# Kernel optimization log

Hardware: AMD Instinct MI355X
Metric: run time of the kernel (lower is better)

## Reference

```python
import jax, jax.numpy as jnp
import numpy as np

HIDDEN = 512
HEADS = 8
HEAD_DIM = HIDDEN // HEADS
INNER = int(HIDDEN * 4.0)
MAX_DIST = 512
LN_EPS = 1e-5


def _layernorm(x, g, b):
    mu = jnp.mean(x, axis=-1, keepdims=True)
    var = jnp.var(x, axis=-1, keepdims=True)
    return (x - mu) * jax.lax.rsqrt(var + LN_EPS) * g + b


def setup_inputs() -> dict:
    key = jax.random.key(0)
    ks = jax.random.split(key, 12)
    B, T = 4, 2048
    s = 0.02
    return {
        "x": jax.random.normal(ks[0], (B, T, HIDDEN), dtype=jnp.float32),
        "w_qkv": jax.random.normal(ks[1], (HIDDEN, 3 * HIDDEN), dtype=jnp.float32) * s,
        "b_qkv": jnp.zeros((3 * HIDDEN,), dtype=jnp.float32),
        "w_out": jax.random.normal(ks[2], (HIDDEN, HIDDEN), dtype=jnp.float32) * s,
        "b_out": jnp.zeros((HIDDEN,), dtype=jnp.float32),
        "ln1_g": jnp.ones((HIDDEN,), dtype=jnp.float32),
        "ln1_b": jnp.zeros((HIDDEN,), dtype=jnp.float32),
        "ln2_g": jnp.ones((HIDDEN,), dtype=jnp.float32),
        "ln2_b": jnp.zeros((HIDDEN,), dtype=jnp.float32),
        "w_mlp1": jax.random.normal(ks[3], (HIDDEN, INNER), dtype=jnp.float32) * s,
        "b_mlp1": jnp.zeros((INNER,), dtype=jnp.float32),
        "w_mlp2": jax.random.normal(ks[4], (INNER, HIDDEN), dtype=jnp.float32) * s,
        "b_mlp2": jnp.zeros((HIDDEN,), dtype=jnp.float32),
        "rel_table": jax.random.normal(ks[5], (2 * MAX_DIST + 1, HEADS), dtype=jnp.float32) * s,
    }


def reference(x, w_qkv, b_qkv, w_out, b_out, ln1_g, ln1_b, ln2_g, ln2_b,
              w_mlp1, b_mlp1, w_mlp2, b_mlp2, rel_table):
    B, T, C = x.shape
    scale = HEAD_DIM ** -0.5
    qkv = x @ w_qkv + b_qkv  # [B,T,3C]
    qkv = qkv.reshape(B, T, 3, HEADS, HEAD_DIM)
    q = qkv[:, :, 0].transpose(0, 2, 1, 3)  # [B,H,T,D]
    k = qkv[:, :, 1].transpose(0, 2, 1, 3)
    v = qkv[:, :, 2].transpose(0, 2, 1, 3)
    logits = jnp.einsum('bhqd,bhkd->bhqk', q, k) * scale
    # relative position bias: clamp(q_pos - k_pos) lookup -> [H,T,T]
    rel = jnp.clip(jnp.arange(T)[:, None] - jnp.arange(T)[None, :], -MAX_DIST, MAX_DIST) + MAX_DIST
    bias = rel_table[rel].transpose(2, 0, 1)  # [H,T,T]
    logits = logits + bias[None]
    attn = jax.nn.softmax(logits, axis=-1)
    out = jnp.einsum('bhqk,bhkd->bhqd', attn, v)
    out = out.transpose(0, 2, 1, 3).reshape(B, T, C)
    out = out @ w_out + b_out
    x = _layernorm(x + out, ln1_g, ln1_b)
    h = jax.nn.gelu(x @ w_mlp1 + b_mlp1, approximate=False)
    mlp_out = h @ w_mlp2 + b_mlp2
    return _layernorm(x + mlp_out, ln2_g, ln2_b)
```

## Files before the change

kernel.cpp:

```cpp
#include <hip/hip_runtime.h>
#include <hip/hip_bf16.h>

using bf16 = __hip_bfloat16;
typedef __attribute__((ext_vector_type(8))) short bf16x8;
typedef __attribute__((ext_vector_type(4))) short bf16x4;
typedef __attribute__((ext_vector_type(4))) float f32x4;

#define HIDDEN 512
#define HEADS 8
#define HDIM 64
#define INNER 2048
#define MAXD 512
#define BB 4
#define TT 2048
#define MM (BB*TT)
#define LOG2E 1.44269504088896340736f

typedef const __attribute__((address_space(1))) unsigned int* gas_u32p;
typedef __attribute__((address_space(3))) unsigned int* las_u32p;

__device__ __forceinline__ void gload_lds16(const void* g, void* l) {
    __builtin_amdgcn_global_load_lds((gas_u32p)g, (las_u32p)l, 16, 0, 0);
}
__device__ __forceinline__ short bfr(float x) {
    return (short)__bfloat16_as_ushort(__float2bfloat16(x));
}
__device__ __forceinline__ float bf2f(short u) {
    return __uint_as_float(((unsigned)(unsigned short)u) << 16);
}

__global__ __launch_bounds__(256) void cast_kernel(const float* __restrict__ in,
                                                   bf16* __restrict__ out) {
    int i = (blockIdx.x * 256 + threadIdx.x) * 4;
    float4 v = *(const float4*)&in[i];
    bf16 o[4] = {__float2bfloat16(v.x), __float2bfloat16(v.y),
                 __float2bfloat16(v.z), __float2bfloat16(v.w)};
    *(bf16x4*)&out[i] = *(bf16x4*)o;
}

__global__ __launch_bounds__(256) void wtrans_kernel(const float* __restrict__ in,
                                                     bf16* __restrict__ out,
                                                     int K, int N) {
    __shared__ float tile[32][33];
    int bx = blockIdx.x;
    int by = blockIdx.y;
    int lx = threadIdx.x & 31, ly = threadIdx.x >> 5;
    #pragma unroll
    for (int i = 0; i < 4; ++i)
        tile[ly + 8*i][lx] = in[(size_t)(by*32 + ly + 8*i) * N + bx*32 + lx];
    __syncthreads();
    #pragma unroll
    for (int i = 0; i < 4; ++i)
        out[(size_t)(bx*32 + ly + 8*i) * K + by*32 + lx] =
            __float2bfloat16(tile[lx][ly + 8*i]);
}

template<int EPI, int BN, int VT, int RESID>
__global__ __launch_bounds__(256) void gemm_kernel(
    const bf16* __restrict__ A, const bf16* __restrict__ BT,
    const float* __restrict__ bias, const void* __restrict__ resid,
    bf16* __restrict__ C, bf16* __restrict__ vt_out,
    int M, int N, int K)
{
    constexpr int NBF = BN / 32;
    constexpr int BBYTES = BN * 64;
    __shared__ __align__(16) bf16 As[2][128*32];
    __shared__ __align__(16) bf16 Bs[2][BN*32];
    const int tid = threadIdx.x;
    const int wid = tid >> 6;
    const int lane = tid & 63;
    const int lhi = lane >> 4, llo = lane & 15;
    const int m0 = blockIdx.x * 128, n0 = blockIdx.y * BN;
    const int wr = wid >> 1, wc = wid & 1;

    const int srow = tid >> 2;
    const int scol = ((tid & 3) ^ ((srow >> 1) & 3)) * 8;
    const bf16* Ap = A + (size_t)(m0 + srow) * K + scol;
    const bf16* Bp = BT + (size_t)(n0 + srow) * K + scol;
    const size_t step64 = (size_t)64 * K;
    const int rsw = (llo >> 1) & 3;

    f32x4 acc[4][NBF] = {};

    gload_lds16(Ap,          (char*)As + tid*16);
    gload_lds16(Ap + step64, (char*)As + 4096 + tid*16);
    gload_lds16(Bp,          (char*)Bs + tid*16);
    if (BN == 128) gload_lds16(Bp + step64, (char*)Bs + 4096 + tid*16);

    const int NK = K >> 5;
    for (int it = 0; it < NK; ++it) {
        const int p = it & 1;
        __syncthreads();
        if (it + 1 < NK) {
            const int k1 = (it + 1) << 5;
            gload_lds16(Ap + k1,          (char*)As + (p^1)*8192 + tid*16);
            gload_lds16(Ap + k1 + step64, (char*)As + (p^1)*8192 + 4096 + tid*16);
            gload_lds16(Bp + k1,          (char*)Bs + (p^1)*BBYTES + tid*16);
            if (BN == 128) gload_lds16(Bp + k1 + step64, (char*)Bs + (p^1)*BBYTES + 4096 + tid*16);
        }
        bf16x8 af[4], bfrg[NBF];
        #pragma unroll
        for (int ar = 0; ar < 4; ++ar)
            af[ar] = *(const bf16x8*)((const char*)As + p*8192 +
                       (64*wr + 16*ar + llo)*64 + ((lhi ^ rsw) << 4));
        #pragma unroll
        for (int bc = 0; bc < NBF; ++bc)
            bfrg[bc] = *(const bf16x8*)((const char*)Bs + p*BBYTES +
                       ((BN/2)*wc + 16*bc + llo)*64 + ((lhi ^ rsw) << 4));
        #pragma unroll
        for (int ar = 0; ar < 4; ++ar)
            #pragma unroll
            for (int bc = 0; bc < NBF; ++bc)
                acc[ar][bc] = __builtin_amdgcn_mfma_f32_16x16x32_bf16(
                    af[ar], bfrg[bc], acc[ar][bc], 0, 0, 0);
    }

    if (VT && n0 >= 1024) {
        #pragma unroll
        for (int ar = 0; ar < 4; ++ar) {
            const int row = m0 + 64*wr + 16*ar + 4*lhi;
            const int bq = row >> 11, t0 = row & 2047;
            #pragma unroll
            for (int bc = 0; bc < NBF; ++bc) {
                const int cv = n0 - 1024 + (BN/2)*wc + 16*bc + llo;
                const int h = cv >> 6, d = cv & 63;
                float bv = bias[n0 + (BN/2)*wc + 16*bc + llo];
                bf16x4 pk = {bfr(acc[ar][bc][0] + bv), bfr(acc[ar][bc][1] + bv),
                             bfr(acc[ar][bc][2] + bv), bfr(acc[ar][bc][3] + bv)};
                *(bf16x4*)&vt_out[(((size_t)(bq*8 + h) * 64 + d) << 11) + t0] = pk;
            }
        }
        return;
    }

    #pragma unroll
    for (int ar = 0; ar < 4; ++ar) {
        #pragma unroll
        for (int j = 0; j < 4; ++j) {
            int row = m0 + 64*wr + 16*ar + 4*lhi + j;
            #pragma unroll
            for (int bc = 0; bc < NBF; ++bc) {
                int col = n0 + (BN/2)*wc + 16*bc + llo;
                float v = acc[ar][bc][j] + bias[col];
                if (RESID == 1)
                    v += ((const float*)resid)[(size_t)row * N + col];
                if (RESID == 2)
                    v += __bfloat162float(((const bf16*)resid)[(size_t)row * N + col]);
                if (EPI == 2) {
                    float u = 0.7978845608028654f * (v + 0.044715f * v * v * v);
                    float e = __builtin_amdgcn_exp2f(u * (2.0f * LOG2E));
                    v = v * (1.0f - 1.0f / (1.0f + e));
                }
                C[(size_t)row * N + col] = __float2bfloat16(v);
            }
        }
    }
}

#define PTN (TT + 128)
__global__ __launch_bounds__(512) void attn_kernel(
    const bf16* __restrict__ qkv,
    const bf16* __restrict__ v_t,
    const float* __restrict__ rel_table,
    bf16* __restrict__ attn_out)
{
    __shared__ __align__(16) bf16 Ks[2][64*64];
    __shared__ __align__(16) bf16 Vs[2][64*64];
    __shared__ __align__(16) bf16 Ps[8][16*64];
    __shared__ float PT[PTN];

    const int qt = blockIdx.x, bh = blockIdx.y;
    const int b = bh >> 3, h = bh & 7;
    const int tid = threadIdx.x, wid = tid >> 6, lane = tid & 63;
    const int lhi = lane >> 4, llo = lane & 15;

    const int lo = qt * 128 - (TT - 1);
    for (int i = tid; i < PTN; i += 512) {
        int idx = min(max(i + lo, -MAXD), MAXD) + MAXD;
        PT[i] = rel_table[(size_t)idx * HEADS + h] * LOG2E;
    }

    const int q0w = qt * 128 + wid * 16;
    const int qb = qt * 128;
    const int q = q0w + llo;
    bf16x8 bq[2];
    #pragma unroll
    for (int kc = 0; kc < 2; ++kc)
        bq[kc] = *(const bf16x8*)&qkv[(size_t)(b*TT + q) * 1536 + h*64 + kc*32 + lhi*8];

    const int so = tid * 16;
    const int r0 = so >> 7;
    const int c0 = (((so & 127) ^ ((r0 & 7) << 4)) >> 1);
    const bf16* kbase = qkv + (size_t)(b*TT) * 1536 + 512 + h*64;
    const bf16* vbase = v_t + (size_t)bh * 64 * TT;

    float accL = 0.f;
    f32x4 accO[4] = {};
    const int pti = wid*16 + llo + (TT - 1);

    gload_lds16(kbase + (size_t)r0 * 1536 + c0, (char*)Ks + so);
    gload_lds16(vbase + (size_t)r0 * TT + c0,   (char*)Vs + so);
    __syncthreads();

    const float cFut  = PT[min(max(-512 - lo, 0), PTN - 1)];
    const float cPast = PT[min(max( 512 - lo, 0), PTN - 1)];

    constexpr int NT = TT / 64;
    for (int kt = 0; kt < NT; ++kt) {
        const int p = kt & 1;
        const int kv0 = kt * 64;
        if (kt) __syncthreads();
        if (kt + 1 < NT) {
            const int kn = kv0 + 64;
            gload_lds16(kbase + (size_t)(kn + r0) * 1536 + c0, (char*)Ks + (p^1)*8192 + so);
            gload_lds16(vbase + (size_t)r0 * TT + kn + c0,     (char*)Vs + (p^1)*8192 + so);
        }
        const char* Kb = (const char*)Ks + p*8192;
        const char* Vb = (const char*)Vs + p*8192;

        f32x4 s[4];
        __builtin_amdgcn_s_setprio(1);
        #pragma unroll
        for (int f = 0; f < 4; ++f) {
            f32x4 a = {};
            const int rr = 16*f + llo;
            #pragma unroll
            for (int kc = 0; kc < 2; ++kc) {
                bf16x8 ak = *(const bf16x8*)(Kb + rr*128 + (((4*kc + lhi) ^ (rr & 7)) << 4));
                a = __builtin_amdgcn_mfma_f32_16x16x32_bf16(ak, bq[kc], a, 0, 0, 0);
            }
            s[f] = a;
        }
        __builtin_amdgcn_s_setprio(0);

        const float sc = 0.125f * LOG2E;
        if (kv0 >= qb + 640) {
            #pragma unroll
            for (int f = 0; f < 4; ++f)
                #pragma unroll
                for (int j = 0; j < 4; ++j)
                    s[f][j] = fmaf(s[f][j], sc, cFut);
        } else if (kv0 + 576 <= qb) {
            #pragma unroll
            for (int f = 0; f < 4; ++f)
                #pragma unroll
                for (int j = 0; j < 4; ++j)
                    s[f][j] = fmaf(s[f][j], sc, cPast);
        } else {
            const int ib = pti - kv0;
            #pragma unroll
            for (int f = 0; f < 4; ++f)
                #pragma unroll
                for (int j = 0; j < 4; ++j)
                    s[f][j] = fmaf(s[f][j], sc, PT[ib - 16*f - 4*lhi - j]);
        }

        float tf[4];
        #pragma unroll
        for (int f = 0; f < 4; ++f) {
            float p0 = __builtin_amdgcn_exp2f(s[f][0]);
            float p1 = __builtin_amdgcn_exp2f(s[f][1]);
            float p2 = __builtin_amdgcn_exp2f(s[f][2]);
            float p3 = __builtin_amdgcn_exp2f(s[f][3]);
            tf[f] = (p0 + p1) + (p2 + p3);
            bf16x4 pk = {bfr(p0), bfr(p1), bfr(p2), bfr(p3)};
            *(bf16x4*)((char*)Ps + wid*2048 + llo*128 +
                       ((f*32 + lhi*8) ^ ((llo & 7) << 4))) = pk;
        }
        accL += (tf[0] + tf[1]) + (tf[2] + tf[3]);

        bf16x8 pf[2];
        #pragma unroll
        for (int kc = 0; kc < 2; ++kc)
            pf[kc] = *(const bf16x8*)((const char*)Ps + wid*2048 + llo*128 +
                                      ((kc*64 + lhi*16) ^ ((llo & 7) << 4)));
        __builtin_amdgcn_s_setprio(1);
        #pragma unroll
        for (int kc = 0; kc < 2; ++kc)
            #pragma unroll
            for (int f = 0; f < 4; ++f) {
                const int rr = 16*f + llo;
                bf16x8 av = *(const bf16x8*)(Vb + rr*128 + (((4*kc + lhi) ^ (rr & 7)) << 4));
                accO[f] = __builtin_amdgcn_mfma_f32_16x16x32_bf16(av, pf[kc], accO[f], 0, 0, 0);
            }
        __builtin_amdgcn_s_setprio(0);
    }

    accL += __shfl_xor(accL, 16, 64);
    accL += __shfl_xor(accL, 32, 64);
    const float rl = 1.0f / accL;
    const int row = b*TT + q;
    #pragma unroll
    for (int f = 0; f < 4; ++f) {
        bf16x4 ov = {bfr(accO[f][0] * rl), bfr(accO[f][1] * rl),
                     bfr(accO[f][2] * rl), bfr(accO[f][3] * rl)};
        *(bf16x4*)&attn_out[(size_t)row * HIDDEN + h*64 + 16*f + 4*lhi] = ov;
    }
}

template<int WB>
__global__ __launch_bounds__(256) void ln_kernel(
    const bf16* __restrict__ in,
    const float* __restrict__ g, const float* __restrict__ bb,
    float* __restrict__ of, bf16* __restrict__ ob)
{
    int row = blockIdx.x * 4 + (threadIdx.x >> 6);
    int lane = threadIdx.x & 63;
    const bf16* pa = in + (size_t)row * HIDDEN + lane * 8;
    bf16x8 v8 = *(const bf16x8*)pa;
    float v[8];
    float s = 0.f, sq = 0.f;
    #pragma unroll
    for (int j = 0; j < 8; ++j) {
        v[j] = bf2f(v8[j]);
        s += v[j]; sq += v[j] * v[j];
    }
    #pragma unroll
    for (int d = 1; d < 64; d <<= 1) {
        s  += __shfl_xor(s,  d, 64);
        sq += __shfl_xor(sq, d, 64);
    }
    float mean = s * (1.f / HIDDEN);
    float var  = sq * (1.f / HIDDEN) - mean * mean;
    float rstd = rsqrtf(var + 1e-5f);
    float o[8];
    #pragma unroll
    for (int j = 0; j < 8; ++j) {
        int col = lane * 8 + j;
        o[j] = (v[j] - mean) * rstd * g[col] + bb[col];
    }
    if (WB) {
        bf16x8 ov;
        #pragma unroll
        for (int j = 0; j < 8; ++j) ov[j] = bfr(o[j]);
        *(bf16x8*)&ob[(size_t)row * HIDDEN + lane * 8] = ov;
    } else {
        float4 o0 = {o[0], o[1], o[2], o[3]};
        float4 o1 = {o[4], o[5], o[6], o[7]};
        *(float4*)&of[(size_t)row * HIDDEN + lane * 8]     = o0;
        *(float4*)&of[(size_t)row * HIDDEN + lane * 8 + 4] = o1;
    }
}

extern "C" void kernel_launch(void* const* d_in, const int* in_sizes, int n_in,
                              void* d_out, int out_size, void* d_ws, size_t ws_size,
                              hipStream_t stream) {
    const float* x     = (const float*)d_in[0];
    const float* w_qkv = (const float*)d_in[1];
    const float* b_qkv = (const float*)d_in[2];
    const float* w_out = (const float*)d_in[3];
    const float* b_out = (const float*)d_in[4];
    const float* ln1_g = (const float*)d_in[5];
    const float* ln1_b = (const float*)d_in[6];
    const float* ln2_g = (const float*)d_in[7];
    const float* ln2_b = (const float*)d_in[8];
    const float* w1    = (const float*)d_in[9];
    const float* b1    = (const float*)d_in[10];
    const float* w2    = (const float*)d_in[11];
    const float* b2    = (const float*)d_in[12];
    const float* rel   = (const float*)d_in[13];
    float* out = (float*)d_out;

    char* ws = (char*)d_ws;
    bf16*  xb     = (bf16*)(ws + 0);
    bf16*  wqkv_t = (bf16*)(ws + 8388608);
    bf16*  wout_t = (bf16*)(ws + 9961472);
    bf16*  w1_t   = (bf16*)(ws + 10485760);
    bf16*  w2_t   = (bf16*)(ws + 12582912);
    bf16*  qkv    = (bf16*)(ws + 14680064);
    bf16*  v_t    = (bf16*)(ws + 39845888);
    bf16*  attn_o = (bf16*)(ws + 48234496);
    bf16*  proj   = (bf16*)(ws + 56623104);
    bf16*  h      = (bf16*)(ws + 14680064);
    bf16*  x1b    = (bf16*)(ws + 90177536);

    cast_kernel<<<MM*HIDDEN/4/256, 256, 0, stream>>>(x, xb);
    wtrans_kernel<<<dim3(1536/32, 512/32),  256, 0, stream>>>(w_qkv, wqkv_t, 512, 1536);
    wtrans_kernel<<<dim3(512/32,  512/32),  256, 0, stream>>>(w_out, wout_t, 512, 512);
    wtrans_kernel<<<dim3(2048/32, 512/32),  256, 0, stream>>>(w1,    w1_t,   512, 2048);
    wtrans_kernel<<<dim3(512/32,  2048/32), 256, 0, stream>>>(w2,    w2_t,   2048, 512);
    gemm_kernel<0,128,1,0><<<dim3(MM/128, 1536/128), 256, 0, stream>>>(
        xb, wqkv_t, b_qkv, nullptr, qkv, v_t, MM, 1536, 512);
    attn_kernel<<<dim3(TT/128, BB*HEADS), 512, 0, stream>>>(qkv, v_t, rel, attn_o);
    gemm_kernel<0,64,0,1><<<dim3(MM/128, 512/64), 256, 0, stream>>>(
        attn_o, wout_t, b_out, x, proj, nullptr, MM, 512, 512);
    ln_kernel<1><<<MM/4, 256, 0, stream>>>(proj, ln1_g, ln1_b, nullptr, x1b);
    gemm_kernel<2,128,0,0><<<dim3(MM/128, 2048/128), 256, 0, stream>>>(
        x1b, w1_t, b1, nullptr, h, nullptr, MM, 2048, 512);
    gemm_kernel<0,64,0,2><<<dim3(MM/128, 512/64), 256, 0, stream>>>(
        h, w2_t, b2, x1b, proj, nullptr, MM, 512, 2048);
    ln_kernel<0><<<MM/4, 256, 0, stream>>>(proj, ln2_g, ln2_b, out, nullptr);
}
```

Baseline: 187.6 us.

## Split attention KV across two wave groups, fuse prep casts into one kernel

The attention kernel now has each wave handle 32 queries instead of 16. The two groups of four waves each process half of every 64-key tile, which reuses each K and V fragment across two query blocks. The partial output and denominator sums from the two groups are merged through shared memory at the end. Separately, the input cast and the four weight transposes are merged into one launch to cut kernel launch overhead. The trade-offs are more registers per thread and an extra shared-memory reduction step.

Result: faster. 177.8 us (median of 2 runs) (-5.3%).

```diff
diff --git a/kernel.cpp b/kernel.cpp
--- a/kernel.cpp
+++ b/kernel.cpp
@@ -29,21 +29,29 @@
     return __uint_as_float(((unsigned)(unsigned short)u) << 16);
 }
 
-__global__ __launch_bounds__(256) void cast_kernel(const float* __restrict__ in,
-                                                   bf16* __restrict__ out) {
-    int i = (blockIdx.x * 256 + threadIdx.x) * 4;
-    float4 v = *(const float4*)&in[i];
-    bf16 o[4] = {__float2bfloat16(v.x), __float2bfloat16(v.y),
-                 __float2bfloat16(v.z), __float2bfloat16(v.w)};
-    *(bf16x4*)&out[i] = *(bf16x4*)o;
-}
-
-__global__ __launch_bounds__(256) void wtrans_kernel(const float* __restrict__ in,
-                                                     bf16* __restrict__ out,
-                                                     int K, int N) {
+__global__ __launch_bounds__(256) void prep_kernel(
+    const float* __restrict__ x, const float* __restrict__ w_qkv,
+    const float* __restrict__ w_out, const float* __restrict__ w1,
+    const float* __restrict__ w2,
+    bf16* __restrict__ xb, bf16* __restrict__ wqkv_t, bf16* __restrict__ wout_t,
+    bf16* __restrict__ w1_t, bf16* __restrict__ w2_t)
+{
     __shared__ float tile[32][33];
-    int bx = blockIdx.x;
-    int by = blockIdx.y;
+    int bid = blockIdx.x;
+    if (bid < 4096) {
+        int i = (bid * 256 + threadIdx.x) * 4;
+        float4 v = *(const float4*)&x[i];
+        bf16 o[4] = {__float2bfloat16(v.x), __float2bfloat16(v.y),
+                     __float2bfloat16(v.z), __float2bfloat16(v.w)};
+        *(bf16x4*)&xb[i] = *(bf16x4*)o;
+        return;
+    }
+    bid -= 4096;
+    const float* in; bf16* out; int K, N, bx, by;
+    if (bid < 768)       { in = w_qkv; out = wqkv_t; K = 512;  N = 1536; bx = bid % 48; by = bid / 48; }
+    else if (bid < 1024) { bid -= 768;  in = w_out; out = wout_t; K = 512;  N = 512;  bx = bid % 16; by = bid / 16; }
+    else if (bid < 2048) { bid -= 1024; in = w1;   out = w1_t;   K = 512;  N = 2048; bx = bid % 64; by = bid / 64; }
+    else                 { bid -= 2048; in = w2;   out = w2_t;   K = 2048; N = 512;  bx = bid % 16; by = bid / 16; }
     int lx = threadIdx.x & 31, ly = threadIdx.x >> 5;
     #pragma unroll
     for (int i = 0; i < 4; ++i)
@@ -164,137 +172,185 @@
     const float* __restrict__ rel_table,
     bf16* __restrict__ attn_out)
 {
-    __shared__ __align__(16) bf16 Ks[2][64*64];
-    __shared__ __align__(16) bf16 Vs[2][64*64];
-    __shared__ __align__(16) bf16 Ps[8][16*64];
-    __shared__ float PT[PTN];
+    __shared__ __align__(16) char smem[49152 + PTN*4];
+    char* KsB = smem;
+    char* VsB = smem + 16384;
+    char* PsB = smem + 32768;
+    float* PT = (float*)(smem + 49152);
 
     const int qt = blockIdx.x, bh = blockIdx.y;
     const int b = bh >> 3, h = bh & 7;
     const int tid = threadIdx.x, wid = tid >> 6, lane = tid & 63;
     const int lhi = lane >> 4, llo = lane & 15;
-
-    const int lo = qt * 128 - (TT - 1);
+    const int gw = wid >> 2;
+    const int wq = wid & 3;
+
+    const int lo = qt*128 - (TT - 1);
     for (int i = tid; i < PTN; i += 512) {
         int idx = min(max(i + lo, -MAXD), MAXD) + MAXD;
         PT[i] = rel_table[(size_t)idx * HEADS + h] * LOG2E;
     }
 
-    const int q0w = qt * 128 + wid * 16;
     const int qb = qt * 128;
-    const int q = q0w + llo;
-    bf16x8 bq[2];
-    #pragma unroll
-    for (int kc = 0; kc < 2; ++kc)
-        bq[kc] = *(const bf16x8*)&qkv[(size_t)(b*TT + q) * 1536 + h*64 + kc*32 + lhi*8];
+    const int q0w = qb + wq * 32;
+    bf16x8 bq[2][2];
+    #pragma unroll
+    for (int qh = 0; qh < 2; ++qh)
+        #pragma unroll
+        for (int kc = 0; kc < 2; ++kc)
+            bq[qh][kc] = *(const bf16x8*)&qkv[(size_t)(b*TT + q0w + qh*16 + llo) * 1536
+                                              + h*64 + kc*32 + lhi*8];
 
     const int so = tid * 16;
-    const int r0 = so >> 7;
-    const int c0 = (((so & 127) ^ ((r0 & 7) << 4)) >> 1);
+    const int kg = so >> 12;
+    const int kr = (so >> 7) & 31;
+    const int kc0 = (((so & 127) ^ ((kr & 7) << 4)) >> 1);
+    const int vd = (so >> 7) & 63;
+    const int vbs = (so & 127) ^ ((vd & 7) << 4);
+    const int vg = vbs >> 6;
+    const int vke = (vbs & 63) >> 1;
+
     const bf16* kbase = qkv + (size_t)(b*TT) * 1536 + 512 + h*64;
     const bf16* vbase = v_t + (size_t)bh * 64 * TT;
 
-    float accL = 0.f;
-    f32x4 accO[4] = {};
-    const int pti = wid*16 + llo + (TT - 1);
-
-    gload_lds16(kbase + (size_t)r0 * 1536 + c0, (char*)Ks + so);
-    gload_lds16(vbase + (size_t)r0 * TT + c0,   (char*)Vs + so);
+    float accL[2] = {};
+    f32x4 accO[2][4] = {};
+
+    gload_lds16(kbase + (size_t)(kg*32 + kr) * 1536 + kc0, KsB + so);
+    gload_lds16(vbase + (size_t)vd * TT + vg*32 + vke,     VsB + so);
     __syncthreads();
 
     const float cFut  = PT[min(max(-512 - lo, 0), PTN - 1)];
     const float cPast = PT[min(max( 512 - lo, 0), PTN - 1)];
-
-    constexpr int NT = TT / 64;
-    for (int kt = 0; kt < NT; ++kt) {
-        const int p = kt & 1;
-        const int kv0 = kt * 64;
-        if (kt) __syncthreads();
-        if (kt + 1 < NT) {
-            const int kn = kv0 + 64;
-            gload_lds16(kbase + (size_t)(kn + r0) * 1536 + c0, (char*)Ks + (p^1)*8192 + so);
-            gload_lds16(vbase + (size_t)r0 * TT + kn + c0,     (char*)Vs + (p^1)*8192 + so);
-        }
-        const char* Kb = (const char*)Ks + p*8192;
-        const char* Vb = (const char*)Vs + p*8192;
-
-        f32x4 s[4];
+    const float sc = 0.125f * LOG2E;
+    const int ibq = wq*32 + llo + (TT - 1) - 4*lhi;
+
+    for (int it = 0; it < 32; ++it) {
+        const int p = it & 1;
+        const int kv0 = it*64 + gw*32;
+        if (it) __syncthreads();
+        if (it + 1 < 32) {
+            const int kn = (it + 1) * 64;
+            gload_lds16(kbase + (size_t)(kn + kg*32 + kr) * 1536 + kc0, KsB + (p^1)*8192 + so);
+            gload_lds16(vbase + (size_t)vd * TT + kn + vg*32 + vke,     VsB + (p^1)*8192 + so);
+        }
+        const char* Kb = KsB + p*8192 + gw*4096;
+        const char* Vb = VsB + p*8192;
+
+        f32x4 s[2][2] = {};
         __builtin_amdgcn_s_setprio(1);
         #pragma unroll
-        for (int f = 0; f < 4; ++f) {
-            f32x4 a = {};
+        for (int f = 0; f < 2; ++f) {
             const int rr = 16*f + llo;
             #pragma unroll
             for (int kc = 0; kc < 2; ++kc) {
                 bf16x8 ak = *(const bf16x8*)(Kb + rr*128 + (((4*kc + lhi) ^ (rr & 7)) << 4));
-                a = __builtin_amdgcn_mfma_f32_16x16x32_bf16(ak, bq[kc], a, 0, 0, 0);
+                #pragma unroll
+                for (int qh = 0; qh < 2; ++qh)
+                    s[qh][f] = __builtin_amdgcn_mfma_f32_16x16x32_bf16(
+                        ak, bq[qh][kc], s[qh][f], 0, 0, 0);
             }
-            s[f] = a;
         }
         __builtin_amdgcn_s_setprio(0);
 
-        const float sc = 0.125f * LOG2E;
-        if (kv0 >= qb + 640) {
-            #pragma unroll
-            for (int f = 0; f < 4; ++f)
+        if (kv0 >= qb + 639) {
+            #pragma unroll
+            for (int qh = 0; qh < 2; ++qh)
+                #pragma unroll
+                for (int f = 0; f < 2; ++f)
+                    #pragma unroll
+                    for (int j = 0; j < 4; ++j)
+                        s[qh][f][j] = fmaf(s[qh][f][j], sc, cFut);
+        } else if (kv0 <= qb - 543) {
+            #pragma unroll
+            for (int qh = 0; qh < 2; ++qh)
+                #pragma unroll
+                for (int f = 0; f < 2; ++f)
+                    #pragma unroll
+                    for (int j = 0; j < 4; ++j)
+                        s[qh][f][j] = fmaf(s[qh][f][j], sc, cPast);
+        } else {
+            const int ib = ibq - kv0;
+            #pragma unroll
+            for (int qh = 0; qh < 2; ++qh)
+                #pragma unroll
+                for (int f = 0; f < 2; ++f)
+                    #pragma unroll
+                    for (int j = 0; j < 4; ++j)
+                        s[qh][f][j] = fmaf(s[qh][f][j], sc, PT[ib + qh*16 - 16*f - j]);
+        }
+
+        #pragma unroll
+        for (int qh = 0; qh < 2; ++qh) {
+            float tf = 0.f;
+            #pragma unroll
+            for (int f = 0; f < 2; ++f) {
+                float p0 = __builtin_amdgcn_exp2f(s[qh][f][0]);
+                float p1 = __builtin_amdgcn_exp2f(s[qh][f][1]);
+                float p2 = __builtin_amdgcn_exp2f(s[qh][f][2]);
+                float p3 = __builtin_amdgcn_exp2f(s[qh][f][3]);
+                tf += (p0 + p1) + (p2 + p3);
+                bf16x4 pk = {bfr(p0), bfr(p1), bfr(p2), bfr(p3)};
+                *(bf16x4*)(PsB + wid*2048 + llo*128 +
+                           ((qh*64 + f*32 + lhi*8) ^ ((llo & 7) << 4))) = pk;
+            }
+            accL[qh] += tf;
+        }
+
+        bf16x8 pf[2];
+        #pragma unroll
+        for (int qh = 0; qh < 2; ++qh)
+            pf[qh] = *(const bf16x8*)(PsB + wid*2048 + llo*128 +
+                                      ((qh*64 + lhi*16) ^ ((llo & 7) << 4)));
+        __builtin_amdgcn_s_setprio(1);
+        #pragma unroll
+        for (int fd = 0; fd < 4; ++fd) {
+            const int rv = 16*fd + llo;
+            bf16x8 av = *(const bf16x8*)(Vb + rv*128 +
+                         ((gw*64 + lhi*16) ^ ((rv & 7) << 4)));
+            #pragma unroll
+            for (int qh = 0; qh < 2; ++qh)
+                accO[qh][fd] = __builtin_amdgcn_mfma_f32_16x16x32_bf16(
+                    av, pf[qh], accO[qh][fd], 0, 0, 0);
+        }
+        __builtin_amdgcn_s_setprio(0);
+    }
+
+    #pragma unroll
+    for (int qh = 0; qh < 2; ++qh) {
+        accL[qh] += __shfl_xor(accL[qh], 16, 64);
+        accL[qh] += __shfl_xor(accL[qh], 32, 64);
+    }
+
+    __syncthreads();
+    float* xbuf = (float*)smem;
+    if (gw == 1) {
+        float* dst = xbuf + (size_t)(wq*64 + lane) * 34;
+        #pragma unroll
+        for (int qh = 0; qh < 2; ++qh)
+            #pragma unroll
+            for (int fd = 0; fd < 4; ++fd)
                 #pragma unroll
                 for (int j = 0; j < 4; ++j)
-                    s[f][j] = fmaf(s[f][j], sc, cFut);
-        } else if (kv0 + 576 <= qb) {
-            #pragma unroll
-            for (int f = 0; f < 4; ++f)
-                #pragma unroll
-                for (int j = 0; j < 4; ++j)
-                    s[f][j] = fmaf(s[f][j], sc, cPast);
-        } else {
-            const int ib = pti - kv0;
-            #pragma unroll
-            for (int f = 0; f < 4; ++f)
-                #pragma unroll
-                for (int j = 0; j < 4; ++j)
-                    s[f][j] = fmaf(s[f][j], sc, PT[ib - 16*f - 4*lhi - j]);
-        }
-
-        float tf[4];
-        #pragma unroll
-        for (int f = 0; f < 4; ++f) {
-            float p0 = __builtin_amdgcn_exp2f(s[f][0]);
-            float p1 = __builtin_amdgcn_exp2f(s[f][1]);
-            float p2 = __builtin_amdgcn_exp2f(s[f][2]);
-            float p3 = __builtin_amdgcn_exp2f(s[f][3]);
-            tf[f] = (p0 + p1) + (p2 + p3);
-            bf16x4 pk = {bfr(p0), bfr(p1), bfr(p2), bfr(p3)};
-            *(bf16x4*)((char*)Ps + wid*2048 + llo*128 +
-                       ((f*32 + lhi*8) ^ ((llo & 7) << 4))) = pk;
-        }
-        accL += (tf[0] + tf[1]) + (tf[2] + tf[3]);
-
-        bf16x8 pf[2];
-        #pragma unroll
-        for (int kc = 0; kc < 2; ++kc)
-            pf[kc] = *(const bf16x8*)((const char*)Ps + wid*2048 + llo*128 +
-                                      ((kc*64 + lhi*16) ^ ((llo & 7) << 4)));
-        __builtin_amdgcn_s_setprio(1);
-        #pragma unroll
-        for (int kc = 0; kc < 2; ++kc)
-            #pragma unroll
-            for (int f = 0; f < 4; ++f) {
-                const int rr = 16*f + llo;
-                bf16x8 av = *(const bf16x8*)(Vb + rr*128 + (((4*kc + lhi) ^ (rr & 7)) << 4));
-                accO[f] = __builtin_amdgcn_mfma_f32_16x16x32_bf16(av, pf[kc], accO[f], 0, 0, 0);
+                    dst[qh*16 + fd*4 + j] = accO[qh][fd][j];
+        dst[32] = accL[0]; dst[33] = accL[1];
+    }
+    __syncthreads();
+    if (gw == 0) {
+        const float* src = xbuf + (size_t)(wq*64 + lane) * 34;
+        #pragma unroll
+        for (int qh = 0; qh < 2; ++qh) {
+            const float rl = 1.0f / (accL[qh] + src[32 + qh]);
+            const int row = b*TT + q0w + qh*16 + llo;
+            #pragma unroll
+            for (int fd = 0; fd < 4; ++fd) {
+                bf16x4 ov = {bfr((accO[qh][fd][0] + src[qh*16 + fd*4 + 0]) * rl),
+                             bfr((accO[qh][fd][1] + src[qh*16 + fd*4 + 1]) * rl),
+                             bfr((accO[qh][fd][2] + src[qh*16 + fd*4 + 2]) * rl),
+                             bfr((accO[qh][fd][3] + src[qh*16 + fd*4 + 3]) * rl)};
+                *(bf16x4*)&attn_out[(size_t)row * HIDDEN + h*64 + 16*fd + 4*lhi] = ov;
             }
-        __builtin_amdgcn_s_setprio(0);
-    }
-
-    accL += __shfl_xor(accL, 16, 64);
-    accL += __shfl_xor(accL, 32, 64);
-    const float rl = 1.0f / accL;
-    const int row = b*TT + q;
-    #pragma unroll
-    for (int f = 0; f < 4; ++f) {
-        bf16x4 ov = {bfr(accO[f][0] * rl), bfr(accO[f][1] * rl),
-                     bfr(accO[f][2] * rl), bfr(accO[f][3] * rl)};
-        *(bf16x4*)&attn_out[(size_t)row * HIDDEN + h*64 + 16*f + 4*lhi] = ov;
+        }
     }
 }
 
@@ -374,11 +430,8 @@
     bf16*  h      = (bf16*)(ws + 14680064);
     bf16*  x1b    = (bf16*)(ws + 90177536);
 
-    cast_kernel<<<MM*HIDDEN/4/256, 256, 0, stream>>>(x, xb);
-    wtrans_kernel<<<dim3(1536/32, 512/32),  256, 0, stream>>>(w_qkv, wqkv_t, 512, 1536);
-    wtrans_kernel<<<dim3(512/32,  512/32),  256, 0, stream>>>(w_out, wout_t, 512, 512);
-    wtrans_kernel<<<dim3(2048/32, 512/32),  256, 0, stream>>>(w1,    w1_t,   512, 2048);
-    wtrans_kernel<<<dim3(512/32,  2048/32), 256, 0, stream>>>(w2,    w2_t,   2048, 512);
+    prep_kernel<<<7168, 256, 0, stream>>>(x, w_qkv, w_out, w1, w2,
+                                          xb, wqkv_t, wout_t, w1_t, w2_t);
     gemm_kernel<0,128,1,0><<<dim3(MM/128, 1536/128), 256, 0, stream>>>(
         xb, wqkv_t, b_qkv, nullptr, qkv, v_t, MM, 1536, 512);
     attn_kernel<<<dim3(TT/128, BB*HEADS), 512, 0, stream>>>(qkv, v_t, rel, attn_o);
```
